# Kernel optimization log

Hardware: AMD Instinct MI355X
Metric: run time of the kernel (lower is better)

Reference implementation:

```python
import jax, jax.numpy as jnp
import numpy as np


def _pool2(x):
    # 2x2 max pool, stride 2 (matches F.max_pool2d(x, 2))
    b, c, h, w = x.shape
    return x.reshape(b, c, h // 2, 2, w // 2, 2).max(axis=(3, 5))


def setup_inputs() -> dict:
    key = jax.random.key(0)
    ks = jax.random.split(key, 6)
    B, C, H, W = 16, 512, 64, 64
    x = jax.random.normal(ks[0], (B, C, H, W), dtype=jnp.float32)
    scale = 0.02
    theta_w = jax.random.normal(ks[1], (C // 8, C), dtype=jnp.float32) * scale
    phi_w = jax.random.normal(ks[2], (C // 8, C), dtype=jnp.float32) * scale
    g_w = jax.random.normal(ks[3], (C // 2, C), dtype=jnp.float32) * scale
    o_w = jax.random.normal(ks[4], (C, C // 2), dtype=jnp.float32) * scale
    # original inits gamma=0; use a nonzero value so output depends on attention path
    gamma = jax.random.normal(ks[5], (), dtype=jnp.float32) * 0.5
    return {"x": x, "theta_w": theta_w, "phi_w": phi_w, "g_w": g_w, "o_w": o_w, "gamma": gamma}


def reference(x, theta_w, phi_w, g_w, o_w, gamma):
    B, C, H, W = x.shape
    HW = H * W
    # 1x1 convs == channel GEMMs
    theta = jnp.einsum('bchw,kc->bkhw', x, theta_w).reshape(B, C // 8, HW).transpose(0, 2, 1)  # [B, HW, C/8]
    phi = _pool2(jnp.einsum('bchw,kc->bkhw', x, phi_w)).reshape(B, C // 8, HW // 4)            # [B, C/8, HW/4]
    beta = jax.nn.softmax(jnp.einsum('bnk,bkm->bnm', theta, phi), axis=-1)                     # [B, HW, HW/4]
    g = _pool2(jnp.einsum('bchw,kc->bkhw', x, g_w)).reshape(B, C // 2, HW // 4)                # [B, C/2, HW/4]
    # g.bmm(beta^T): contract over pooled positions m -> [B, C/2, HW]
    o_in = jnp.einsum('bcm,bnm->bcn', g, beta).reshape(B, C // 2, H, W)
    o = jnp.einsum('bchw,kc->bkhw', o_in, o_w)                                                 # [B, C, H, W]
    return gamma * o + x
```

## Files before the change

kernel.cpp:

```cpp
#include <hip/hip_runtime.h>

#define B_   16
#define C_   512
#define HW_  4096
#define M_   1024

typedef __attribute__((ext_vector_type(8))) short bf16x8;
typedef __attribute__((ext_vector_type(4))) float f32x4;

static __device__ __forceinline__ unsigned short f2bf(float f) {
    union { float f; unsigned u; } v; v.f = f;
    unsigned r = v.u + 0x7fffu + ((v.u >> 16) & 1u);
    return (unsigned short)(r >> 16);
}
static __device__ __forceinline__ float bf2f(unsigned short h) {
    union { unsigned u; float f; } v; v.u = ((unsigned)h) << 16;
    return v.f;
}
static __device__ __forceinline__ void gload_lds16(const void* g, void* l) {
    __builtin_amdgcn_global_load_lds(
        (const __attribute__((address_space(1))) unsigned int*)g,
        (__attribute__((address_space(3))) unsigned int*)l, 16, 0, 0);
}

__global__ __launch_bounds__(256) void k_weights(
    const float* __restrict__ thw, const float* __restrict__ phw,
    const float* __restrict__ gw,  const float* __restrict__ ow,
    unsigned short* __restrict__ Wb, unsigned short* __restrict__ oWb) {
    int i = blockIdx.x * 256 + threadIdx.x;
    if (i < 32768)            Wb[i] = f2bf(thw[i]);
    else if (i < 65536)       Wb[i] = f2bf(phw[i - 32768]);
    else if (i < 196608)      Wb[i] = f2bf(gw[i - 65536]);
    i -= 196608;
    if (i >= 0 && i < 131072) oWb[i] = f2bf(ow[i]);
}

__global__ __launch_bounds__(256) void k_transpose_x(
    const float* __restrict__ x, unsigned short* __restrict__ xT) {
    __shared__ float tile[64][65];
    int b = blockIdx.z, c0 = blockIdx.y * 64, hw0 = blockIdx.x * 64;
    const float* xb = x + ((size_t)b * C_ + c0) * HW_ + hw0;
    int t = threadIdx.x;
    int r = t >> 4, c4 = (t & 15) * 4;
#pragma unroll
    for (int k = 0; k < 4; k++) {
        int row = r + k * 16;
        float4 v = *reinterpret_cast<const float4*>(xb + (size_t)row * HW_ + c4);
        tile[row][c4 + 0] = v.x; tile[row][c4 + 1] = v.y;
        tile[row][c4 + 2] = v.z; tile[row][c4 + 3] = v.w;
    }
    __syncthreads();
    unsigned short* o = xT + ((size_t)b * HW_ + hw0) * C_ + c0;
#pragma unroll
    for (int k = 0; k < 4; k++) {
        int hwr = r + k * 16;
        ushort4 u;
        u.x = f2bf(tile[c4 + 0][hwr]); u.y = f2bf(tile[c4 + 1][hwr]);
        u.z = f2bf(tile[c4 + 2][hwr]); u.w = f2bf(tile[c4 + 3][hwr]);
        *reinterpret_cast<ushort4*>(o + (size_t)hwr * C_ + c4) = u;
    }
}

__global__ __launch_bounds__(256, 4) void k_proj(
    const unsigned short* __restrict__ xT, const unsigned short* __restrict__ Wb,
    unsigned short* __restrict__ P_all, unsigned short* __restrict__ theta_n) {
    __shared__ unsigned short As[128 * 64];
    __shared__ unsigned short Bs[128 * 64];

    int b = blockIdx.z, mt = blockIdx.y, hw0 = blockIdx.x * 128;
    int tid = threadIdx.x, w = tid >> 6, lane = tid & 63;
    int l15 = lane & 15, q = lane >> 4;
    int wr = w >> 1, wc = w & 1;

    const unsigned short* Ab = Wb + (size_t)(mt * 128) * 512;
    const unsigned short* Bb = xT + ((size_t)b * HW_ + hw0) * 512;
    int trow = tid >> 3, tch = tid & 7;

    f32x4 acc[4][4] = {};
    for (int ks = 0; ks < 8; ks++) {
        int k0 = ks * 64;
        if (ks) __syncthreads();
#pragma unroll
        for (int i = 0; i < 4; i++) {
            int row = i * 32 + trow;
            int ch = tch ^ (row & 7);
            gload_lds16(Ab + (size_t)row * 512 + k0 + ch * 8, &As[(i * 256 + w * 64) * 8]);
        }
#pragma unroll
        for (int i = 0; i < 4; i++) {
            int row = i * 32 + trow;
            int ch = tch ^ (row & 7);
            gload_lds16(Bb + (size_t)row * 512 + k0 + ch * 8, &Bs[(i * 256 + w * 64) * 8]);
        }
        __syncthreads();
#pragma unroll
        for (int kk = 0; kk < 2; kk++) {
            bf16x8 af[4], bfr[4];
#pragma unroll
            for (int mi = 0; mi < 4; mi++) {
                int row = wr * 64 + mi * 16 + l15;
                int ch = (kk * 4 + q) ^ (row & 7);
                af[mi] = *(const bf16x8*)&As[row * 64 + ch * 8];
            }
#pragma unroll
            for (int ni = 0; ni < 4; ni++) {
                int row = wc * 64 + ni * 16 + l15;
                int ch = (kk * 4 + q) ^ (row & 7);
                bfr[ni] = *(const bf16x8*)&Bs[row * 64 + ch * 8];
            }
#pragma unroll
            for (int mi = 0; mi < 4; mi++)
#pragma unroll
                for (int ni = 0; ni < 4; ni++)
                    acc[mi][ni] = __builtin_amdgcn_mfma_f32_16x16x32_bf16(
                        af[mi], bfr[ni], acc[mi][ni], 0, 0, 0);
        }
    }

    if (mt == 0 && wr == 0) {
#pragma unroll
        for (int mi = 0; mi < 4; mi++)
#pragma unroll
            for (int ni = 0; ni < 4; ni++) {
                ushort4 u;
                u.x = f2bf(acc[mi][ni][0]); u.y = f2bf(acc[mi][ni][1]);
                u.z = f2bf(acc[mi][ni][2]); u.w = f2bf(acc[mi][ni][3]);
                int hw = hw0 + wc * 64 + ni * 16 + l15;
                *reinterpret_cast<ushort4*>(
                    theta_n + ((size_t)b * HW_ + hw) * 64 + mi * 16 + q * 4) = u;
            }
    } else {
        int rbase = mt * 128 + wr * 64;
#pragma unroll
        for (int mi = 0; mi < 4; mi++)
#pragma unroll
            for (int ni = 0; ni < 4; ni++)
#pragma unroll
                for (int j = 0; j < 4; j++) {
                    int r = rbase + mi * 16 + q * 4 + j;
                    P_all[((size_t)b * 384 + r) * HW_ + hw0 + wc * 64 + ni * 16 + l15] =
                        f2bf(acc[mi][ni][j]);
                }
    }
}

__global__ __launch_bounds__(256) void k_pool_phi(
    const unsigned short* __restrict__ P_all, unsigned short* __restrict__ phi_p) {
    int idx = blockIdx.x * 256 + threadIdx.x;
    int b = idx >> 12, m = (idx >> 2) & 1023, kg = idx & 3;
    int hw00 = (m >> 5) * 128 + (m & 31) * 2;
    const unsigned short* src = P_all + ((size_t)b * 384 + 64) * HW_;
    unsigned short* dst = phi_p + ((size_t)b * M_ + m) * 64;
    for (int k = kg * 16; k < kg * 16 + 16; k++) {
        const unsigned short* r = src + (size_t)k * HW_ + hw00;
        float v = fmaxf(fmaxf(bf2f(r[0]), bf2f(r[1])), fmaxf(bf2f(r[64]), bf2f(r[65])));
        dst[k] = f2bf(v);
    }
}

__global__ __launch_bounds__(256) void k_pool_g(
    const unsigned short* __restrict__ P_all, unsigned short* __restrict__ g_p) {
    int b = blockIdx.x, c = blockIdx.y;
    unsigned short* dst = g_p + ((size_t)b * 272 + c) * M_ + threadIdx.x * 4;
    if (c >= 256) {
        unsigned short val = (c == 256) ? (unsigned short)0x3F80u : (unsigned short)0;
        ushort4 u; u.x = val; u.y = val; u.z = val; u.w = val;
        *reinterpret_cast<ushort4*>(dst) = u;
        return;
    }
    const unsigned short* src = P_all + ((size_t)b * 384 + 128 + c) * HW_;
    ushort4 u;
    unsigned short tmp[4];
#pragma unroll
    for (int i = 0; i < 4; i++) {
        int m = threadIdx.x * 4 + i;
        int hw00 = (m >> 5) * 128 + (m & 31) * 2;
        const unsigned short* r = src + hw00;
        float v = fmaxf(fmaxf(bf2f(r[0]), bf2f(r[1])), fmaxf(bf2f(r[64]), bf2f(r[65])));
        tmp[i] = f2bf(v);
    }
    u.x = tmp[0]; u.y = tmp[1]; u.z = tmp[2]; u.w = tmp[3];
    *reinterpret_cast<ushort4*>(dst) = u;
}

__global__ __launch_bounds__(512, 4) void k_attn(
    const unsigned short* __restrict__ theta_n, const unsigned short* __restrict__ phi_p,
    const unsigned short* __restrict__ g_p, unsigned short* __restrict__ o_in) {
    __shared__ unsigned short phi_s[64 * 64];
    __shared__ unsigned short g_s[272 * 64];
    __shared__ unsigned short p_lds[8][16][88];

    int b = blockIdx.y, n0 = blockIdx.x * 128;
    int tid = threadIdx.x, w = tid >> 6, lane = tid & 63;
    int l15 = lane & 15, q = lane >> 4;
    int nw = n0 + w * 16;

    const unsigned short* th = theta_n + ((size_t)b * HW_ + nw + l15) * 64 + q * 8;
    bf16x8 a0 = *(const bf16x8*)(th);
    bf16x8 a1 = *(const bf16x8*)(th + 32);

    const unsigned short* phib = phi_p + (size_t)b * M_ * 64;
    const unsigned short* gb   = g_p   + (size_t)b * 272 * M_;

    int sw = l15 & 7;

    f32x4 acc[17] = {};
    for (int mc = 0; mc < 16; mc++) {
        int m0 = mc * 64;
        __syncthreads();
        {
            int p = tid;
            int row = p >> 3, ch = (p & 7) ^ (row & 7);
            gload_lds16(phib + (size_t)(m0 + row) * 64 + ch * 8, &phi_s[w * 512]);
        }
#pragma unroll
        for (int it = 0; it < 5; it++) {
            int s = w + it * 8;
            if (s < 34) {
                int row = s * 8 + (lane >> 3);
                int ch = (lane & 7) ^ (row & 7);
                gload_lds16(gb + (size_t)row * M_ + m0 + ch * 8, &g_s[s * 512]);
            }
        }
        __syncthreads();

#pragma unroll
        for (int f = 0; f < 4; f++) {
            const unsigned short* pr = &phi_s[(f * 16 + l15) * 64];
            bf16x8 b0 = *(const bf16x8*)(pr + (q ^ sw) * 8);
            bf16x8 b1 = *(const bf16x8*)(pr + ((q + 4) ^ sw) * 8);
            f32x4 s = {};
            s = __builtin_amdgcn_mfma_f32_16x16x32_bf16(a0, b0, s, 0, 0, 0);
            s = __builtin_amdgcn_mfma_f32_16x16x32_bf16(a1, b1, s, 0, 0, 0);
#pragma unroll
            for (int j = 0; j < 4; j++)
                p_lds[w][q * 4 + j][f * 16 + l15] = f2bf(__expf(s[j]));
        }
        bf16x8 p0 = *(const bf16x8*)&p_lds[w][l15][q * 8];
        bf16x8 p1 = *(const bf16x8*)&p_lds[w][l15][32 + q * 8];
#pragma unroll
        for (int cf = 0; cf < 17; cf++) {
            const unsigned short* gr = &g_s[(cf * 16 + l15) * 64];
            bf16x8 g0 = *(const bf16x8*)(gr + (q ^ sw) * 8);
            bf16x8 g1 = *(const bf16x8*)(gr + ((q + 4) ^ sw) * 8);
            acc[cf] = __builtin_amdgcn_mfma_f32_16x16x32_bf16(p0, g0, acc[cf], 0, 0, 0);
            acc[cf] = __builtin_amdgcn_mfma_f32_16x16x32_bf16(p1, g1, acc[cf], 0, 0, 0);
        }
    }

    float dinv[4];
#pragma unroll
    for (int j = 0; j < 4; j++) {
        float d = __shfl(acc[16][j], (lane & 48), 64);
        dinv[j] = 1.0f / d;
    }
#pragma unroll
    for (int cf = 0; cf < 16; cf++)
#pragma unroll
        for (int j = 0; j < 4; j++)
            o_in[((size_t)b * HW_ + nw + q * 4 + j) * 256 + cf * 16 + l15] =
                f2bf(acc[cf][j] * dinv[j]);
}

__global__ __launch_bounds__(256, 4) void k_oproj(
    const unsigned short* __restrict__ o_in, const unsigned short* __restrict__ oWb,
    const float* __restrict__ x, const float* __restrict__ gamma_p,
    float* __restrict__ out) {
    __shared__ unsigned short As[128 * 64];
    __shared__ unsigned short Bs[128 * 64];

    int b = blockIdx.z, mt = blockIdx.y, hw0 = blockIdx.x * 128;
    int tid = threadIdx.x, w = tid >> 6, lane = tid & 63;
    int l15 = lane & 15, q = lane >> 4;
    int wr = w >> 1, wc = w & 1;

    const unsigned short* Ab = oWb + (size_t)(mt * 128) * 256;
    const unsigned short* Bb = o_in + ((size_t)b * HW_ + hw0) * 256;
    int trow = tid >> 3, tch = tid & 7;

    f32x4 acc[4][4] = {};
    for (int ks = 0; ks < 4; ks++) {
        int k0 = ks * 64;
        if (ks) __syncthreads();
#pragma unroll
        for (int i = 0; i < 4; i++) {
            int row = i * 32 + trow;
            int ch = tch ^ (row & 7);
            gload_lds16(Ab + (size_t)row * 256 + k0 + ch * 8, &As[(i * 256 + w * 64) * 8]);
        }
#pragma unroll
        for (int i = 0; i < 4; i++) {
            int row = i * 32 + trow;
            int ch = tch ^ (row & 7);
            gload_lds16(Bb + (size_t)row * 256 + k0 + ch * 8, &Bs[(i * 256 + w * 64) * 8]);
        }
        __syncthreads();
#pragma unroll
        for (int kk = 0; kk < 2; kk++) {
            bf16x8 af[4], bfr[4];
#pragma unroll
            for (int mi = 0; mi < 4; mi++) {
                int row = wr * 64 + mi * 16 + l15;
                int ch = (kk * 4 + q) ^ (row & 7);
                af[mi] = *(const bf16x8*)&As[row * 64 + ch * 8];
            }
#pragma unroll
            for (int ni = 0; ni < 4; ni++) {
                int row = wc * 64 + ni * 16 + l15;
                int ch = (kk * 4 + q) ^ (row & 7);
                bfr[ni] = *(const bf16x8*)&Bs[row * 64 + ch * 8];
            }
#pragma unroll
            for (int mi = 0; mi < 4; mi++)
#pragma unroll
                for (int ni = 0; ni < 4; ni++)
                    acc[mi][ni] = __builtin_amdgcn_mfma_f32_16x16x32_bf16(
                        af[mi], bfr[ni], acc[mi][ni], 0, 0, 0);
        }
    }

    float gam = *gamma_p;
    int rbase = mt * 128 + wr * 64;
#pragma unroll
    for (int mi = 0; mi < 4; mi++)
#pragma unroll
        for (int ni = 0; ni < 4; ni++)
#pragma unroll
            for (int j = 0; j < 4; j++) {
                int r = rbase + mi * 16 + q * 4 + j;
                size_t idx = ((size_t)b * C_ + r) * HW_ + hw0 + wc * 64 + ni * 16 + l15;
                out[idx] = gam * acc[mi][ni][j] + x[idx];
            }
}

extern "C" void kernel_launch(void* const* d_in, const int* in_sizes, int n_in,
                              void* d_out, int out_size, void* d_ws, size_t ws_size,
                              hipStream_t stream) {
    const float* x     = (const float*)d_in[0];
    const float* thw   = (const float*)d_in[1];
    const float* phw   = (const float*)d_in[2];
    const float* gw    = (const float*)d_in[3];
    const float* ow    = (const float*)d_in[4];
    const float* gamma = (const float*)d_in[5];
    float* out = (float*)d_out;

    char* ws = (char*)d_ws;
    unsigned short* xT   = (unsigned short*)(ws + 0);
    unsigned short* Wb   = (unsigned short*)(ws + 67108864);
    unsigned short* oWb  = (unsigned short*)(ws + 67502080);
    unsigned short* Pall = (unsigned short*)(ws + 67764224);
    unsigned short* thn  = (unsigned short*)(ws + 118095872);
    unsigned short* phip = (unsigned short*)(ws + 126484480);
    unsigned short* gp   = (unsigned short*)(ws + 128581632);
    unsigned short* oin  = Pall;

    hipLaunchKernelGGL(k_weights, dim3(1280), dim3(256), 0, stream, thw, phw, gw, ow, Wb, oWb);
    hipLaunchKernelGGL(k_transpose_x, dim3(64, 8, 16), dim3(256), 0, stream, x, xT);
    hipLaunchKernelGGL(k_proj, dim3(32, 3, 16), dim3(256), 0, stream, xT, Wb, Pall, thn);
    hipLaunchKernelGGL(k_pool_phi, dim3(256), dim3(256), 0, stream, Pall, phip);
    hipLaunchKernelGGL(k_pool_g, dim3(16, 272), dim3(256), 0, stream, Pall, gp);
    hipLaunchKernelGGL(k_attn, dim3(32, 16), dim3(512), 0, stream, thn, phip, gp, oin);
    hipLaunchKernelGGL(k_oproj, dim3(32, 4, 16), dim3(256), 0, stream, oin, oWb, x, gamma, out);
}
```

Measured before the change: 233.7 us.

## Fuse 2x2 max-pooling into projection GEMM epilogue via LDS staging

The projection GEMM now stages its bf16 output tile in shared memory (padded stride) and does the theta store, phi pooling and g pooling directly in its epilogue. This removes the separate pool kernels and the round trip of the full unpooled P_all buffer through global memory. The constant ones/zeros rows of g_p move into the weight-conversion kernel. The output projection also stages its tile through LDS so the gamma*o+x epilogue does coalesced float4 loads and stores, at the cost of extra LDS traffic, barriers, and rounding the result to bf16 before the residual add.

```diff
diff --git a/kernel.cpp b/kernel.cpp
--- a/kernel.cpp
+++ b/kernel.cpp
@@ -4,6 +4,7 @@
 #define C_   512
 #define HW_  4096
 #define M_   1024
+#define TPAD 136
 
 typedef __attribute__((ext_vector_type(8))) short bf16x8;
 typedef __attribute__((ext_vector_type(4))) float f32x4;
@@ -26,13 +27,21 @@
 __global__ __launch_bounds__(256) void k_weights(
     const float* __restrict__ thw, const float* __restrict__ phw,
     const float* __restrict__ gw,  const float* __restrict__ ow,
-    unsigned short* __restrict__ Wb, unsigned short* __restrict__ oWb) {
+    unsigned short* __restrict__ Wb, unsigned short* __restrict__ oWb,
+    unsigned short* __restrict__ g_p) {
     int i = blockIdx.x * 256 + threadIdx.x;
-    if (i < 32768)            Wb[i] = f2bf(thw[i]);
-    else if (i < 65536)       Wb[i] = f2bf(phw[i - 32768]);
-    else if (i < 196608)      Wb[i] = f2bf(gw[i - 65536]);
-    i -= 196608;
-    if (i >= 0 && i < 131072) oWb[i] = f2bf(ow[i]);
+    if (i < 32768)        Wb[i] = f2bf(thw[i]);
+    else if (i < 65536)   Wb[i] = f2bf(phw[i - 32768]);
+    else if (i < 196608)  Wb[i] = f2bf(gw[i - 65536]);
+    else if (i < 327680)  oWb[i - 196608] = f2bf(ow[i - 196608]);
+    else if (i < 589824) {
+        int i2 = i - 327680;
+        int b = i2 >> 14;
+        int r = (i2 >> 10) & 15;
+        int m = i2 & 1023;
+        g_p[((size_t)b * 272 + 256 + r) * M_ + m] =
+            (r == 0) ? (unsigned short)0x3F80u : (unsigned short)0;
+    }
 }
 
 __global__ __launch_bounds__(256) void k_transpose_x(
@@ -63,11 +72,14 @@
 
 __global__ __launch_bounds__(256, 4) void k_proj(
     const unsigned short* __restrict__ xT, const unsigned short* __restrict__ Wb,
-    unsigned short* __restrict__ P_all, unsigned short* __restrict__ theta_n) {
-    __shared__ unsigned short As[128 * 64];
-    __shared__ unsigned short Bs[128 * 64];
-
-    int b = blockIdx.z, mt = blockIdx.y, hw0 = blockIdx.x * 128;
+    unsigned short* __restrict__ theta_n, unsigned short* __restrict__ phi_p,
+    unsigned short* __restrict__ g_p) {
+    __shared__ unsigned short smem[128 * TPAD];
+    unsigned short* As = smem;
+    unsigned short* Bs = smem + 8192;
+
+    int b = blockIdx.z, mt = blockIdx.y, bx = blockIdx.x;
+    int hw0 = bx * 128;
     int tid = threadIdx.x, w = tid >> 6, lane = tid & 63;
     int l15 = lane & 15, q = lane >> 4;
     int wr = w >> 1, wc = w & 1;
@@ -117,70 +129,58 @@
         }
     }
 
-    if (mt == 0 && wr == 0) {
-#pragma unroll
-        for (int mi = 0; mi < 4; mi++)
-#pragma unroll
-            for (int ni = 0; ni < 4; ni++) {
-                ushort4 u;
-                u.x = f2bf(acc[mi][ni][0]); u.y = f2bf(acc[mi][ni][1]);
-                u.z = f2bf(acc[mi][ni][2]); u.w = f2bf(acc[mi][ni][3]);
-                int hw = hw0 + wc * 64 + ni * 16 + l15;
-                *reinterpret_cast<ushort4*>(
-                    theta_n + ((size_t)b * HW_ + hw) * 64 + mi * 16 + q * 4) = u;
-            }
+    __syncthreads();
+#pragma unroll
+    for (int mi = 0; mi < 4; mi++)
+#pragma unroll
+        for (int ni = 0; ni < 4; ni++) {
+            int col = wc * 64 + ni * 16 + l15;
+            int row = wr * 64 + mi * 16 + q * 4;
+            ushort4 u;
+            u.x = f2bf(acc[mi][ni][0]); u.y = f2bf(acc[mi][ni][1]);
+            u.z = f2bf(acc[mi][ni][2]); u.w = f2bf(acc[mi][ni][3]);
+            *reinterpret_cast<ushort4*>(&smem[col * TPAD + row]) = u;
+        }
+    __syncthreads();
+
+    if (mt == 0) {
+        int hw_l = tid >> 1, kh = (tid & 1) * 32;
+        const unsigned short* srcp = &smem[hw_l * TPAD + kh];
+        unsigned short* dstp = theta_n + ((size_t)b * HW_ + hw0 + hw_l) * 64 + kh;
+#pragma unroll
+        for (int i = 0; i < 4; i++)
+            *reinterpret_cast<uint4*>(dstp + i * 8) =
+                *reinterpret_cast<const uint4*>(srcp + i * 8);
+        int pc = tid & 63, mg = tid >> 6;
+#pragma unroll
+        for (int j = 0; j < 8; j++) {
+            int m_l = mg * 8 + j, w_ = m_l * 2;
+            float v0 = bf2f(smem[(w_)      * TPAD + 64 + pc]);
+            float v1 = bf2f(smem[(w_ + 1)  * TPAD + 64 + pc]);
+            float v2 = bf2f(smem[(64 + w_) * TPAD + 64 + pc]);
+            float v3 = bf2f(smem[(65 + w_) * TPAD + 64 + pc]);
+            float v = fmaxf(fmaxf(v0, v1), fmaxf(v2, v3));
+            phi_p[((size_t)b * M_ + bx * 32 + m_l) * 64 + pc] = f2bf(v);
+        }
     } else {
-        int rbase = mt * 128 + wr * 64;
-#pragma unroll
-        for (int mi = 0; mi < 4; mi++)
-#pragma unroll
-            for (int ni = 0; ni < 4; ni++)
-#pragma unroll
-                for (int j = 0; j < 4; j++) {
-                    int r = rbase + mi * 16 + q * 4 + j;
-                    P_all[((size_t)b * 384 + r) * HW_ + hw0 + wc * 64 + ni * 16 + l15] =
-                        f2bf(acc[mi][ni][j]);
-                }
-    }
-}
-
-__global__ __launch_bounds__(256) void k_pool_phi(
-    const unsigned short* __restrict__ P_all, unsigned short* __restrict__ phi_p) {
-    int idx = blockIdx.x * 256 + threadIdx.x;
-    int b = idx >> 12, m = (idx >> 2) & 1023, kg = idx & 3;
-    int hw00 = (m >> 5) * 128 + (m & 31) * 2;
-    const unsigned short* src = P_all + ((size_t)b * 384 + 64) * HW_;
-    unsigned short* dst = phi_p + ((size_t)b * M_ + m) * 64;
-    for (int k = kg * 16; k < kg * 16 + 16; k++) {
-        const unsigned short* r = src + (size_t)k * HW_ + hw00;
-        float v = fmaxf(fmaxf(bf2f(r[0]), bf2f(r[1])), fmaxf(bf2f(r[64]), bf2f(r[65])));
-        dst[k] = f2bf(v);
-    }
-}
-
-__global__ __launch_bounds__(256) void k_pool_g(
-    const unsigned short* __restrict__ P_all, unsigned short* __restrict__ g_p) {
-    int b = blockIdx.x, c = blockIdx.y;
-    unsigned short* dst = g_p + ((size_t)b * 272 + c) * M_ + threadIdx.x * 4;
-    if (c >= 256) {
-        unsigned short val = (c == 256) ? (unsigned short)0x3F80u : (unsigned short)0;
-        ushort4 u; u.x = val; u.y = val; u.z = val; u.w = val;
-        *reinterpret_cast<ushort4*>(dst) = u;
-        return;
-    }
-    const unsigned short* src = P_all + ((size_t)b * 384 + 128 + c) * HW_;
-    ushort4 u;
-    unsigned short tmp[4];
-#pragma unroll
-    for (int i = 0; i < 4; i++) {
-        int m = threadIdx.x * 4 + i;
-        int hw00 = (m >> 5) * 128 + (m & 31) * 2;
-        const unsigned short* r = src + hw00;
-        float v = fmaxf(fmaxf(bf2f(r[0]), bf2f(r[1])), fmaxf(bf2f(r[64]), bf2f(r[65])));
-        tmp[i] = f2bf(v);
-    }
-    u.x = tmp[0]; u.y = tmp[1]; u.z = tmp[2]; u.w = tmp[3];
-    *reinterpret_cast<ushort4*>(dst) = u;
+        int lr = tid & 127, half = tid >> 7;
+        int gc = (mt - 1) * 128 + lr;
+        unsigned short* dst = g_p + ((size_t)b * 272 + gc) * M_ + bx * 32 + half * 16;
+        unsigned short tmp[16];
+#pragma unroll
+        for (int i = 0; i < 16; i++) {
+            int w_ = (half * 16 + i) * 2;
+            float v0 = bf2f(smem[(w_)      * TPAD + lr]);
+            float v1 = bf2f(smem[(w_ + 1)  * TPAD + lr]);
+            float v2 = bf2f(smem[(64 + w_) * TPAD + lr]);
+            float v3 = bf2f(smem[(65 + w_) * TPAD + lr]);
+            tmp[i] = f2bf(fmaxf(fmaxf(v0, v1), fmaxf(v2, v3)));
+        }
+#pragma unroll
+        for (int i = 0; i < 4; i++)
+            *reinterpret_cast<ushort4*>(dst + i * 4) =
+                *reinterpret_cast<const ushort4*>(&tmp[i * 4]);
+    }
 }
 
 __global__ __launch_bounds__(512, 4) void k_attn(
@@ -266,8 +266,9 @@
     const unsigned short* __restrict__ o_in, const unsigned short* __restrict__ oWb,
     const float* __restrict__ x, const float* __restrict__ gamma_p,
     float* __restrict__ out) {
-    __shared__ unsigned short As[128 * 64];
-    __shared__ unsigned short Bs[128 * 64];
+    __shared__ unsigned short smem[128 * TPAD];
+    unsigned short* As = smem;
+    unsigned short* Bs = smem + 8192;
 
     int b = blockIdx.z, mt = blockIdx.y, hw0 = blockIdx.x * 128;
     int tid = threadIdx.x, w = tid >> 6, lane = tid & 63;
@@ -319,18 +320,34 @@
         }
     }
 
+    __syncthreads();
+#pragma unroll
+    for (int mi = 0; mi < 4; mi++)
+#pragma unroll
+        for (int ni = 0; ni < 4; ni++) {
+            int col = wc * 64 + ni * 16 + l15;
+            int rb = wr * 64 + mi * 16 + q * 4;
+#pragma unroll
+            for (int j = 0; j < 4; j++)
+                smem[(rb + j) * TPAD + col] = f2bf(acc[mi][ni][j]);
+        }
+    __syncthreads();
+
     float gam = *gamma_p;
-    int rbase = mt * 128 + wr * 64;
-#pragma unroll
-    for (int mi = 0; mi < 4; mi++)
-#pragma unroll
-        for (int ni = 0; ni < 4; ni++)
-#pragma unroll
-            for (int j = 0; j < 4; j++) {
-                int r = rbase + mi * 16 + q * 4 + j;
-                size_t idx = ((size_t)b * C_ + r) * HW_ + hw0 + wc * 64 + ni * 16 + l15;
-                out[idx] = gam * acc[mi][ni][j] + x[idx];
-            }
+    int sub = tid >> 5, p32 = tid & 31;
+#pragma unroll
+    for (int p = 0; p < 16; p++) {
+        int row = p * 8 + sub;
+        ushort4 v = *reinterpret_cast<const ushort4*>(&smem[row * TPAD + p32 * 4]);
+        size_t idx = ((size_t)b * C_ + mt * 128 + row) * HW_ + hw0 + p32 * 4;
+        float4 xv = *reinterpret_cast<const float4*>(x + idx);
+        float4 o;
+        o.x = gam * bf2f(v.x) + xv.x;
+        o.y = gam * bf2f(v.y) + xv.y;
+        o.z = gam * bf2f(v.z) + xv.z;
+        o.w = gam * bf2f(v.w) + xv.w;
+        *reinterpret_cast<float4*>(out + idx) = o;
+    }
 }
 
 extern "C" void kernel_launch(void* const* d_in, const int* in_sizes, int n_in,
@@ -348,17 +365,14 @@
     unsigned short* xT   = (unsigned short*)(ws + 0);
     unsigned short* Wb   = (unsigned short*)(ws + 67108864);
     unsigned short* oWb  = (unsigned short*)(ws + 67502080);
-    unsigned short* Pall = (unsigned short*)(ws + 67764224);
+    unsigned short* oin  = (unsigned short*)(ws + 67764224);
     unsigned short* thn  = (unsigned short*)(ws + 118095872);
     unsigned short* phip = (unsigned short*)(ws + 126484480);
     unsigned short* gp   = (unsigned short*)(ws + 128581632);
-    unsigned short* oin  = Pall;
-
-    hipLaunchKernelGGL(k_weights, dim3(1280), dim3(256), 0, stream, thw, phw, gw, ow, Wb, oWb);
+
+    hipLaunchKernelGGL(k_weights, dim3(2304), dim3(256), 0, stream, thw, phw, gw, ow, Wb, oWb, gp);
     hipLaunchKernelGGL(k_transpose_x, dim3(64, 8, 16), dim3(256), 0, stream, x, xT);
-    hipLaunchKernelGGL(k_proj, dim3(32, 3, 16), dim3(256), 0, stream, xT, Wb, Pall, thn);
-    hipLaunchKernelGGL(k_pool_phi, dim3(256), dim3(256), 0, stream, Pall, phip);
-    hipLaunchKernelGGL(k_pool_g, dim3(16, 272), dim3(256), 0, stream, Pall, gp);
+    hipLaunchKernelGGL(k_proj, dim3(32, 3, 16), dim3(256), 0, stream, xT, Wb, thn, phip, gp);
     hipLaunchKernelGGL(k_attn, dim3(32, 16), dim3(512), 0, stream, thn, phip, gp, oin);
     hipLaunchKernelGGL(k_oproj, dim3(32, 4, 16), dim3(256), 0, stream, oin, oWb, x, gamma, out);
 }
```

Result: faster. 193.6 us (-17.2%).
